# Kernel optimization log

Measured on AMD Instinct MI355X. Metric: run time of the kernel, lower is better.

The kernel has to match this reference:

```python
import jax, jax.numpy as jnp
from jax import lax
import numpy as np
import math

B, T, D_IN, H, L, NDIR = 32, 512, 1024, 512, 2, 2


def setup_inputs() -> dict:
    key = jax.random.key(0)
    ks = jax.random.split(key, 5)
    std = 1.0 / math.sqrt(H)  # torch init: uniform(-std, std)
    u = lambda k, shape: jax.random.uniform(k, shape, jnp.float32, -std, std)
    return {
        "x": jax.random.normal(ks[0], (B, T, D_IN), jnp.float32),
        "Wx": u(ks[1], (L, NDIR, D_IN, 4 * H)),   # x2h weight (in, 4H)
        "bx": u(ks[2], (L, NDIR, 4 * H)),
        "Wh": u(ks[3], (L, NDIR, H, 4 * H)),      # h2h weight (H, 4H)
        "bh": u(ks[4], (L, NDIR, 4 * H)),
    }


def _lstm_dir(xs, Wx, bx, Wh, bh):
    """xs: [T,B,Din]; returns hs [T,B,H], (hT, cT)."""
    # precompute input projection for all timesteps (one big GEMM)
    gx = jnp.einsum('tbd,dg->tbg', xs, Wx) + bx + bh  # [T,B,4H]
    h0 = jnp.zeros((xs.shape[1], Wh.shape[0]), xs.dtype)

    def step(carry, gx_t):
        h, c = carry
        gates = gx_t + h @ Wh  # [B,4H]
        i, f, g, o = jnp.split(gates, 4, axis=-1)  # torch chunk order: i,f,g,o
        i = jax.nn.sigmoid(i)
        f = jax.nn.sigmoid(f)
        g = jnp.tanh(g)
        o = jax.nn.sigmoid(o)
        c = c * f + i * g
        h = o * jnp.tanh(c)
        return (h, c), h

    (hT, cT), hs = lax.scan(step, (h0, h0), gx)
    return hs, hT, cT


def reference(x, Wx, bx, Wh, bh):
    # x: [B,T,D_IN] (batch_first) -> time-major
    inputs = jnp.swapaxes(x, 0, 1)  # [T,B,D]
    h_list, c_list = [], []
    for layer in range(L):
        outs_dirs = []
        for d in range(NDIR):
            xs = inputs if d == 0 else inputs[::-1]
            hs, hT, cT = _lstm_dir(xs, Wx[layer, d], bx[layer, d], Wh[layer, d], bh[layer, d])
            outs_dirs.append(hs if d == 0 else hs[::-1])
            h_list.append(hT)
            c_list.append(cT)
        inputs = jnp.concatenate(outs_dirs, axis=-1)  # [T,B,2H] (dropout=0 / eval)
    output = jnp.swapaxes(inputs, 0, 1)  # [B,T,2H]
    h_n = jnp.stack(h_list)  # [L*NDIR, B, H]
    c_n = jnp.stack(c_list)
    return output, h_n, c_n
```

## Files before the change

### kernel.cpp

```cpp
#include <hip/hip_runtime.h>
#include <hip/hip_bf16.h>

#define DEV __device__ __forceinline__

typedef __bf16 bf16;
typedef __bf16 bf16x8 __attribute__((ext_vector_type(8)));
typedef float f32x4 __attribute__((ext_vector_type(4)));
typedef int i32x4 __attribute__((ext_vector_type(4)));
typedef unsigned int u32;
typedef unsigned long long u64;

#define BB 32
#define TT 512
#define DIN 1024
#define HH 512
#define G4 2048
#define MM (TT*BB)
#define TAGMAGIC 0x5A000000u

DEV float sigmf(float x){ return 1.0f/(1.0f + __expf(-x)); }
DEV float tanhfast(float x){ return 1.0f - 2.0f/(__expf(2.0f*x)+1.0f); }

DEV void gload16(const void* g, void* l){
  __builtin_amdgcn_global_load_lds((const __attribute__((address_space(1))) void*)g,
                                   (__attribute__((address_space(3))) void*)l, 16, 0, 0);
}

DEV i32x4 cload16(const void* p){
  i32x4 v;
  asm volatile("global_load_dwordx4 %0, %1, off sc0 sc1"
               : "=&v"(v) : "v"(p) : "memory");
  return v;
}
DEV void cstore16(void* p, i32x4 v){
  asm volatile("global_store_dwordx4 %0, %1, off sc0 sc1"
               :: "v"(p), "v"(v) : "memory");
}
DEV void waitvm0(){ asm volatile("s_waitcnt vmcnt(0)" ::: "memory"); }

__global__ void k_dbg(float* out, float v){ out[0] = v; }

__global__ void k_prep_bias(const float* __restrict__ bx, const float* __restrict__ bh,
                            float* __restrict__ bsum){
  int gid = blockIdx.x*256 + threadIdx.x;
  if (gid < 4*G4) bsum[gid] = bx[gid] + bh[gid];
}

__global__ void k_xswz(const float* __restrict__ x, bf16* __restrict__ xs){
  int gid = blockIdx.x*256 + threadIdx.x;
  int r = gid >> 7, kc = gid & 127;
  int b = r & 31, t = r >> 5;
  const float* px = x + ((size_t)b*TT + t)*DIN + kc*8;
  float4 v0 = *(const float4*)px;
  float4 v1 = *(const float4*)(px+4);
  bf16x8 o;
  o[0]=(bf16)v0.x; o[1]=(bf16)v0.y; o[2]=(bf16)v0.z; o[3]=(bf16)v0.w;
  o[4]=(bf16)v1.x; o[5]=(bf16)v1.y; o[6]=(bf16)v1.z; o[7]=(bf16)v1.w;
  *(bf16x8*)(xs + (size_t)r*DIN + ((kc ^ (r&7))<<3)) = o;
}

__global__ void k_twx(const float* __restrict__ Wx, bf16* __restrict__ Wxt){
  int ld = blockIdx.z;
  int k0 = blockIdx.x*64, n0 = blockIdx.y*64;
  const float* in = Wx + (size_t)ld*DIN*G4;
  bf16* outp = Wxt + (size_t)ld*G4*DIN;
  __shared__ float tile[64][68];
  int tid = threadIdx.x;
  #pragma unroll
  for (int rr=0; rr<4; rr++){
    int row = rr*16 + (tid>>4); int c4 = (tid&15)*4;
    float4 v = *(const float4*)(in + (size_t)(k0+row)*G4 + n0 + c4);
    *(float4*)&tile[row][c4] = v;
  }
  __syncthreads();
  #pragma unroll
  for (int uu=0; uu<2; uu++){
    int u = uu*256 + tid;
    int nn = u>>3, ck = u&7;
    bf16x8 o;
    #pragma unroll
    for (int j=0;j<8;j++) o[j] = (bf16)tile[ck*8+j][nn];
    int ncol = n0 + nn;
    int kcg = (k0>>3) + ck;
    *(bf16x8*)(outp + (size_t)ncol*DIN + ((size_t)(kcg ^ (ncol&7))<<3)) = o;
  }
}

__global__ void k_twh(const float* __restrict__ Wh, bf16* __restrict__ Whb){
  int ld = blockIdx.z;
  int k0 = blockIdx.x*64, n0 = blockIdx.y*64;
  const float* in = Wh + (size_t)ld*HH*G4;
  bf16* outp = Whb + (size_t)ld*G4*HH;
  __shared__ float tile[64][68];
  int tid = threadIdx.x;
  #pragma unroll
  for (int rr=0; rr<4; rr++){
    int row = rr*16 + (tid>>4); int c4 = (tid&15)*4;
    float4 v = *(const float4*)(in + (size_t)(k0+row)*G4 + n0 + c4);
    *(float4*)&tile[row][c4] = v;
  }
  __syncthreads();
  #pragma unroll
  for (int uu=0; uu<2; uu++){
    int u = uu*256 + tid;
    int nn = u>>3, ck = u&7;
    bf16x8 o;
    #pragma unroll
    for (int j=0;j<8;j++) o[j] = (bf16)tile[ck*8+j][nn];
    int n = n0 + nn;
    int q = n >> 9, rem = n & 511;
    int s = rem >> 4, wq = (rem >> 2) & 3, hcv = rem & 3;
    int cc = s*64 + wq*16 + q*4 + hcv;
    *(bf16x8*)(outp + (size_t)cc*HH + k0 + ck*8) = o;
  }
}

template<typename GXT>
__launch_bounds__(256, 1)
__global__ void k_gemm(const bf16* __restrict__ A, const bf16* __restrict__ Bw,
                       const float* __restrict__ bias, GXT* __restrict__ out){
  int d = blockIdx.z;
  const bf16* Bp = Bw + (size_t)d*G4*DIN;
  const float* bp = bias + d*G4;
  GXT* op = out + (size_t)d*MM*G4;
  int n0 = blockIdx.x*128, r0 = blockIdx.y*128;
  int tid = threadIdx.x, lane = tid&63, w = tid>>6;
  __shared__ __align__(16) bf16 ldsA[128*64];
  __shared__ __align__(16) bf16 ldsB[128*64];
  f32x4 acc[4][4];
  #pragma unroll
  for (int i=0;i<4;i++)
    #pragma unroll
    for (int j=0;j<4;j++) acc[i][j] = (f32x4){0.f,0.f,0.f,0.f};
  int wm = w>>1, wn = w&1;
  for (int kt=0; kt<16; kt++){
    __syncthreads();
    #pragma unroll
    for (int p=0;p<4;p++){
      int seg = p*4 + w;
      int row = seg*8 + (lane>>3);
      int cch = lane&7;
      gload16(A  + (size_t)(r0+row)*DIN + kt*64 + cch*8, ldsA + seg*512);
      gload16(Bp + (size_t)(n0+row)*DIN + kt*64 + cch*8, ldsB + seg*512);
    }
    __syncthreads();
    #pragma unroll
    for (int ks=0; ks<2; ks++){
      bf16x8 af[4], bf_[4];
      #pragma unroll
      for (int at=0; at<4; at++){
        int row = wm*64 + at*16 + (lane&15);
        int ch = (ks*4 + (lane>>4)) ^ (row&7);
        af[at] = *(const bf16x8*)(ldsA + row*64 + ch*8);
      }
      #pragma unroll
      for (int bt=0; bt<4; bt++){
        int col = wn*64 + bt*16 + (lane&15);
        int ch = (ks*4 + (lane>>4)) ^ (col&7);
        bf_[bt] = *(const bf16x8*)(ldsB + col*64 + ch*8);
      }
      #pragma unroll
      for (int at=0; at<4; at++)
        #pragma unroll
        for (int bt=0; bt<4; bt++)
          acc[at][bt] = __builtin_amdgcn_mfma_f32_16x16x32_bf16(af[at], bf_[bt], acc[at][bt], 0,0,0);
    }
  }
  float bv[4];
  #pragma unroll
  for (int bt=0;bt<4;bt++) bv[bt] = bp[n0 + wn*64 + bt*16 + (lane&15)];
  #pragma unroll
  for (int at=0; at<4; at++)
    #pragma unroll
    for (int bt=0; bt<4; bt++)
      #pragma unroll
      for (int rg=0; rg<4; rg++){
        int row = r0 + wm*64 + at*16 + (lane>>4)*4 + rg;
        int col = n0 + wn*64 + bt*16 + (lane&15);
        op[(size_t)row*G4 + col] = (GXT)(acc[at][bt][rg] + bv[bt]);
      }
}

template<typename GXT>
__launch_bounds__(256, 1)
__global__ void k_rec(const bf16* __restrict__ Whb, const GXT* __restrict__ gx,
                      char* __restrict__ hbT,
                      bf16* __restrict__ out0, float* __restrict__ dout,
                      float* __restrict__ hn, float* __restrict__ cn, int layer, int dir0){
  int tid = threadIdx.x, lane = tid&63, w = tid>>6;
  int dl = blockIdx.x >> 5, s = blockIdx.x & 31;
  int d = dir0 + dl;
  __shared__ __align__(16) bf16 hA[32*512];
  __shared__ __align__(8) unsigned short hP[4*128];
  const bf16* Wp = Whb + ((size_t)d*G4 + s*64 + w*16 + (lane&15))*HH;
  bf16x8 bfr[16];
  #pragma unroll
  for (int kk=0; kk<16; kk++) bfr[kk] = *(const bf16x8*)(Wp + kk*32 + (lane>>4)*8);
  float cst[2][4] = {{0,0,0,0},{0,0,0,0}};
  const GXT* gxD = gx + (size_t)dl*MM*G4;
  const u32 tagbase = TAGMAGIC + (u32)((layer*2 + d)*TT);
  int q = (lane>>2)&3, hc = lane&3;
  int colg = q*HH + s*16 + w*4 + hc;
  int m0 = lane&15;
  bool hi = (q >= 2), odd = (q & 1);

  for (int t=0; t<TT; t++){
    int tt = d ? (TT-1-t) : t;
    GXT gxr[2][4];
    {
      const GXT* gp = gxD + (size_t)tt*BB*G4 + colg;
      #pragma unroll
      for (int mt=0; mt<2; mt++)
        #pragma unroll
        for (int rg=0; rg<4; rg++)
          gxr[mt][rg] = gp[(size_t)(mt*16 + (lane>>4)*4 + rg)*G4];
    }
    f32x4 acc0 = {0.f,0.f,0.f,0.f}, acc1 = {0.f,0.f,0.f,0.f};
    if (t > 0){
      const char* sT = hbT + ((size_t)(dl*2 + ((t-1)&1)) << 16);
      u32 want = tagbase + (u32)t;
      i32x4 u[16];
      #pragma unroll
      for (int i=0;i<16;i++){ int g = i*256 + tid; u[i] = cload16(sT + ((size_t)g<<4)); }
      waitvm0();
      __builtin_amdgcn_sched_barrier(0);
      while (true){
        bool bad = false;
        #pragma unroll
        for (int i=0;i<16;i++) bad |= ((u32)u[i].z != want);
        if (!__any(bad)) break;
        __builtin_amdgcn_s_sleep(1);
        #pragma unroll
        for (int i=0;i<16;i++) if ((u32)u[i].z != want){ int g = i*256 + tid; u[i] = cload16(sT + ((size_t)g<<4)); }
        waitvm0();
        __builtin_amdgcn_sched_barrier(0);
      }
      __syncthreads();
      #pragma unroll
      for (int i=0;i<16;i++){
        int g = i*256 + tid; int b = g>>7, cu = g&127;
        u64 dat = ((u64)(u32)u[i].y << 32) | (u32)u[i].x;
        *(u64*)((char*)hA + b*1024 + ((((cu>>1) ^ (b&7)))<<4) + (cu&1)*8) = dat;
      }
      __syncthreads();
      #pragma unroll
      for (int kk=0; kk<16; kk++){
        int ch = (kk*4 + (lane>>4)) ^ (m0&7);
        bf16x8 a0 = *(const bf16x8*)(hA + m0*HH + ch*8);
        bf16x8 a1 = *(const bf16x8*)(hA + (m0+16)*HH + ch*8);
        acc0 = __builtin_amdgcn_mfma_f32_16x16x32_bf16(a0, bfr[kk], acc0, 0,0,0);
        acc1 = __builtin_amdgcn_mfma_f32_16x16x32_bf16(a1, bfr[kk], acc1, 0,0,0);
      }
    }
    #pragma unroll
    for (int mt=0; mt<2; mt++){
      #pragma unroll
      for (int rg=0; rg<4; rg++){
        float gpre = (mt ? acc1[rg] : acc0[rg]) + (float)gxr[mt][rg];
        float x4  = __shfl_xor(gpre, 4);
        float x8  = __shfl_xor(gpre, 8);
        float x12 = __shfl_xor(gpre, 12);
        float a04 = odd ? x4 : gpre,  b04 = odd ? gpre : x4;
        float a812 = odd ? x12 : x8,  b812 = odd ? x8 : x12;
        float ig = hi ? a812 : a04;
        float fg = hi ? b812 : b04;
        float gg = hi ? a04 : a812;
        float og = hi ? b04 : b812;
        float iv = sigmf(ig), fv = sigmf(fg), gv = tanhfast(gg), ov = sigmf(og);
        float c = cst[mt][rg]*fv + iv*gv;
        cst[mt][rg] = c;
        float hvv = ov * tanhfast(c);
        if (q == 0){
          int b = mt*16 + (lane>>4)*4 + rg;
          hP[w*128 + b*4 + hc] = __builtin_bit_cast(unsigned short, (bf16)hvv);
          if (layer == 1)
            __builtin_nontemporal_store(hvv,
              dout + ((size_t)(b*TT + tt))*(2*HH) + d*HH + s*16 + w*4 + hc);
          if (t == TT-1)
            hn[((size_t)((layer*2+d)*BB + b))*HH + s*16 + w*4 + hc] = hvv;
        }
      }
    }
    if (t == TT-1 && q == 0){
      #pragma unroll
      for (int mt=0; mt<2; mt++)
        #pragma unroll
        for (int rg=0; rg<4; rg++){
          int b = mt*16 + (lane>>4)*4 + rg;
          cn[((size_t)((layer*2+d)*BB + b))*HH + s*16 + w*4 + hc] = cst[mt][rg];
        }
    }
    if (lane < 32){
      u64 d8 = *(const u64*)(hP + w*128 + lane*4);
      if (t < TT-1){
        char* dT = hbT + ((size_t)(dl*2 + (t&1)) << 16);
        i32x4 unit;
        unit.x = (int)(u32)(d8 & 0xffffffffu);
        unit.y = (int)(u32)(d8 >> 32);
        unit.z = (int)(tagbase + (u32)t + 1u);
        unit.w = 0;
        cstore16(dT + ((size_t)(lane*128 + s*4 + w) << 4), unit);
      }
      if (layer == 0){
        int r = tt*BB + lane;
        int c = d*64 + s*2 + (w>>1);
        *(u64*)(out0 + (size_t)r*DIN + (size_t)(c ^ (r&7))*8 + (w&1)*4) = d8;
      }
    }
  }
}

extern "C" void kernel_launch(void* const* d_in, const int* in_sizes, int n_in,
                              void* d_out, int out_size, void* d_ws, size_t ws_size,
                              hipStream_t stream){
  const float* x  = (const float*)d_in[0];
  const float* Wx = (const float*)d_in[1];
  const float* bx = (const float*)d_in[2];
  const float* Wh = (const float*)d_in[3];
  const float* bh = (const float*)d_in[4];
  float* outp = (float*)d_out;
  char* ws = (char*)d_ws;

  const size_t szWxt  = (size_t)4*G4*DIN*2;
  const size_t szWhb  = (size_t)4*G4*HH*2;
  const size_t szBsum = (size_t)4*G4*4;
  const size_t szXO   = (size_t)MM*DIN*2;
  const size_t szHbT  = (size_t)2*2*4096*16;

  int mode = -1;
  size_t oWxt=0,oWhb=0,oBsum=0,oXO=0,oOut0=0,oHbT=0,oGx=0;
  for (int m=0; m<3 && mode<0; m++){
    size_t off = 0;
    auto take = [&](size_t b)->size_t{ size_t r = off; off = (off + b + 255) & ~(size_t)255; return r; };
    oWxt = take(szWxt); oWhb = take(szWhb); oBsum = take(szBsum);
    oXO  = take(szXO);
    oOut0 = (m==2) ? take(szXO) : oXO;
    oHbT = take(szHbT);
    size_t gxb = (m==0) ? (size_t)2*MM*G4*4 : (m==1) ? (size_t)2*MM*G4*2 : (size_t)MM*G4*2;
    oGx = take(gxb);
    if (off <= ws_size) mode = m;
  }
  if (mode < 0){
    k_dbg<<<1, 1, 0, stream>>>(outp, (float)((double)ws_size / 1048576.0));
    return;
  }

  bf16* Wxt  = (bf16*)(ws + oWxt);
  bf16* Whb  = (bf16*)(ws + oWhb);
  float* bsum= (float*)(ws + oBsum);
  bf16* xo   = (bf16*)(ws + oXO);
  bf16* out0 = (bf16*)(ws + oOut0);
  char* hbT  = ws + oHbT;
  void* gxp  = (void*)(ws + oGx);

  float* hn = outp + (size_t)BB*TT*2*HH;
  float* cn = hn + (size_t)4*BB*HH;

  hipMemsetAsync(hbT, 0, szHbT, stream);
  k_prep_bias<<<32, 256, 0, stream>>>(bx, bh, bsum);
  k_xswz<<<(MM*128)/256, 256, 0, stream>>>(x, xo);
  k_twx<<<dim3(16,32,4), 256, 0, stream>>>(Wx, Wxt);
  k_twh<<<dim3(8,32,4), 256, 0, stream>>>(Wh, Whb);

  if (mode == 0){
    float* gx = (float*)gxp;
    for (int layer=0; layer<2; layer++){
      k_gemm<float><<<dim3(16,128,2), 256, 0, stream>>>(xo, Wxt + (size_t)layer*2*G4*DIN,
                                                        bsum + layer*2*G4, gx);
      k_rec<float><<<64, 256, 0, stream>>>(Whb + (size_t)layer*2*G4*HH, gx, hbT,
                                           out0, outp, hn, cn, layer, 0);
    }
  } else if (mode == 1){
    bf16* gx = (bf16*)gxp;
    for (int layer=0; layer<2; layer++){
      k_gemm<bf16><<<dim3(16,128,2), 256, 0, stream>>>(xo, Wxt + (size_t)layer*2*G4*DIN,
                                                       bsum + layer*2*G4, gx);
      k_rec<bf16><<<64, 256, 0, stream>>>(Whb + (size_t)layer*2*G4*HH, gx, hbT,
                                          out0, outp, hn, cn, layer, 0);
    }
  } else {
    bf16* gx = (bf16*)gxp;
    for (int layer=0; layer<2; layer++){
      const bf16* A = layer ? out0 : xo;
      for (int dd=0; dd<2; dd++){
        k_gemm<bf16><<<dim3(16,128,1), 256, 0, stream>>>(A, Wxt + (size_t)(layer*2+dd)*G4*DIN,
                                                         bsum + (layer*2+dd)*G4, gx);
        k_rec<bf16><<<32, 256, 0, stream>>>(Whb + (size_t)layer*2*G4*HH, gx, hbT,
                                            out0, outp, hn, cn, layer, dd);
      }
    }
  }
}
```

Before: 5.624 ms.

## Process both LSTM directions in one recurrent block, interleaved per timestep

The recurrent kernel now launches 32 blocks, each handling one slice of both directions, instead of 64 blocks with one direction each. Per timestep a block spins on direction 0's h exchange, computes and publishes it, then does the same for direction 1. Ideally each direction's inter-block sync latency is hidden behind the other direction's compute. This doubles the weight registers per thread and serializes both directions' work within one CU. The fallback mode that ran one direction per launch is also removed.

```diff
diff --git a/kernel.cpp b/kernel.cpp
--- a/kernel.cpp
+++ b/kernel.cpp
@@ -183,128 +183,136 @@
 
 template<typename GXT>
 __launch_bounds__(256, 1)
-__global__ void k_rec(const bf16* __restrict__ Whb, const GXT* __restrict__ gx,
-                      char* __restrict__ hbT,
-                      bf16* __restrict__ out0, float* __restrict__ dout,
-                      float* __restrict__ hn, float* __restrict__ cn, int layer, int dir0){
+__global__ void k_rec2(const bf16* __restrict__ Whb, const GXT* __restrict__ gx,
+                       char* __restrict__ hbT,
+                       bf16* __restrict__ out0, float* __restrict__ dout,
+                       float* __restrict__ hn, float* __restrict__ cn, int layer){
   int tid = threadIdx.x, lane = tid&63, w = tid>>6;
-  int dl = blockIdx.x >> 5, s = blockIdx.x & 31;
-  int d = dir0 + dl;
+  int s = blockIdx.x;
   __shared__ __align__(16) bf16 hA[32*512];
   __shared__ __align__(8) unsigned short hP[4*128];
-  const bf16* Wp = Whb + ((size_t)d*G4 + s*64 + w*16 + (lane&15))*HH;
-  bf16x8 bfr[16];
-  #pragma unroll
-  for (int kk=0; kk<16; kk++) bfr[kk] = *(const bf16x8*)(Wp + kk*32 + (lane>>4)*8);
-  float cst[2][4] = {{0,0,0,0},{0,0,0,0}};
-  const GXT* gxD = gx + (size_t)dl*MM*G4;
-  const u32 tagbase = TAGMAGIC + (u32)((layer*2 + d)*TT);
+  bf16x8 bfr[2][16];
+  #pragma unroll
+  for (int d=0; d<2; d++){
+    const bf16* Wp = Whb + ((size_t)d*G4 + s*64 + w*16 + (lane&15))*HH;
+    #pragma unroll
+    for (int kk=0; kk<16; kk++) bfr[d][kk] = *(const bf16x8*)(Wp + kk*32 + (lane>>4)*8);
+  }
+  float cst[2][2][4] = {};
   int q = (lane>>2)&3, hc = lane&3;
   int colg = q*HH + s*16 + w*4 + hc;
   int m0 = lane&15;
   bool hi = (q >= 2), odd = (q & 1);
+  u32 tagb0 = TAGMAGIC + (u32)((layer*2+0)*TT);
+  u32 tagb1 = TAGMAGIC + (u32)((layer*2+1)*TT);
 
   for (int t=0; t<TT; t++){
-    int tt = d ? (TT-1-t) : t;
-    GXT gxr[2][4];
-    {
-      const GXT* gp = gxD + (size_t)tt*BB*G4 + colg;
+    GXT gxr[2][2][4];
+    #pragma unroll
+    for (int d=0; d<2; d++){
+      int tt = d ? (TT-1-t) : t;
+      const GXT* gp = gx + (size_t)d*MM*G4 + (size_t)tt*BB*G4 + colg;
       #pragma unroll
       for (int mt=0; mt<2; mt++)
         #pragma unroll
         for (int rg=0; rg<4; rg++)
-          gxr[mt][rg] = gp[(size_t)(mt*16 + (lane>>4)*4 + rg)*G4];
-    }
-    f32x4 acc0 = {0.f,0.f,0.f,0.f}, acc1 = {0.f,0.f,0.f,0.f};
-    if (t > 0){
-      const char* sT = hbT + ((size_t)(dl*2 + ((t-1)&1)) << 16);
-      u32 want = tagbase + (u32)t;
-      i32x4 u[16];
-      #pragma unroll
-      for (int i=0;i<16;i++){ int g = i*256 + tid; u[i] = cload16(sT + ((size_t)g<<4)); }
-      waitvm0();
-      __builtin_amdgcn_sched_barrier(0);
-      while (true){
-        bool bad = false;
-        #pragma unroll
-        for (int i=0;i<16;i++) bad |= ((u32)u[i].z != want);
-        if (!__any(bad)) break;
-        __builtin_amdgcn_s_sleep(1);
-        #pragma unroll
-        for (int i=0;i<16;i++) if ((u32)u[i].z != want){ int g = i*256 + tid; u[i] = cload16(sT + ((size_t)g<<4)); }
+          gxr[d][mt][rg] = gp[(size_t)(mt*16 + (lane>>4)*4 + rg)*G4];
+    }
+    #pragma unroll
+    for (int d=0; d<2; d++){
+      int tt = d ? (TT-1-t) : t;
+      u32 tagbase = d ? tagb1 : tagb0;
+      f32x4 acc0 = {0.f,0.f,0.f,0.f}, acc1 = {0.f,0.f,0.f,0.f};
+      if (t > 0){
+        const char* sT = hbT + ((size_t)(d*2 + ((t-1)&1)) << 16);
+        u32 want = tagbase + (u32)t;
+        i32x4 u[16];
+        #pragma unroll
+        for (int i=0;i<16;i++){ int g = i*256 + tid; u[i] = cload16(sT + ((size_t)g<<4)); }
         waitvm0();
         __builtin_amdgcn_sched_barrier(0);
-      }
-      __syncthreads();
-      #pragma unroll
-      for (int i=0;i<16;i++){
-        int g = i*256 + tid; int b = g>>7, cu = g&127;
-        u64 dat = ((u64)(u32)u[i].y << 32) | (u32)u[i].x;
-        *(u64*)((char*)hA + b*1024 + ((((cu>>1) ^ (b&7)))<<4) + (cu&1)*8) = dat;
-      }
-      __syncthreads();
-      #pragma unroll
-      for (int kk=0; kk<16; kk++){
-        int ch = (kk*4 + (lane>>4)) ^ (m0&7);
-        bf16x8 a0 = *(const bf16x8*)(hA + m0*HH + ch*8);
-        bf16x8 a1 = *(const bf16x8*)(hA + (m0+16)*HH + ch*8);
-        acc0 = __builtin_amdgcn_mfma_f32_16x16x32_bf16(a0, bfr[kk], acc0, 0,0,0);
-        acc1 = __builtin_amdgcn_mfma_f32_16x16x32_bf16(a1, bfr[kk], acc1, 0,0,0);
-      }
-    }
-    #pragma unroll
-    for (int mt=0; mt<2; mt++){
-      #pragma unroll
-      for (int rg=0; rg<4; rg++){
-        float gpre = (mt ? acc1[rg] : acc0[rg]) + (float)gxr[mt][rg];
-        float x4  = __shfl_xor(gpre, 4);
-        float x8  = __shfl_xor(gpre, 8);
-        float x12 = __shfl_xor(gpre, 12);
-        float a04 = odd ? x4 : gpre,  b04 = odd ? gpre : x4;
-        float a812 = odd ? x12 : x8,  b812 = odd ? x8 : x12;
-        float ig = hi ? a812 : a04;
-        float fg = hi ? b812 : b04;
-        float gg = hi ? a04 : a812;
-        float og = hi ? b04 : b812;
-        float iv = sigmf(ig), fv = sigmf(fg), gv = tanhfast(gg), ov = sigmf(og);
-        float c = cst[mt][rg]*fv + iv*gv;
-        cst[mt][rg] = c;
-        float hvv = ov * tanhfast(c);
-        if (q == 0){
-          int b = mt*16 + (lane>>4)*4 + rg;
-          hP[w*128 + b*4 + hc] = __builtin_bit_cast(unsigned short, (bf16)hvv);
-          if (layer == 1)
-            __builtin_nontemporal_store(hvv,
-              dout + ((size_t)(b*TT + tt))*(2*HH) + d*HH + s*16 + w*4 + hc);
-          if (t == TT-1)
-            hn[((size_t)((layer*2+d)*BB + b))*HH + s*16 + w*4 + hc] = hvv;
-        }
-      }
-    }
-    if (t == TT-1 && q == 0){
-      #pragma unroll
-      for (int mt=0; mt<2; mt++)
+        while (true){
+          bool bad = false;
+          #pragma unroll
+          for (int i=0;i<16;i++) bad |= ((u32)u[i].z != want);
+          if (!__any(bad)) break;
+          __builtin_amdgcn_s_sleep(1);
+          #pragma unroll
+          for (int i=0;i<16;i++) if ((u32)u[i].z != want){ int g = i*256 + tid; u[i] = cload16(sT + ((size_t)g<<4)); }
+          waitvm0();
+          __builtin_amdgcn_sched_barrier(0);
+        }
+        __syncthreads();
+        #pragma unroll
+        for (int i=0;i<16;i++){
+          int g = i*256 + tid; int b = g>>7, cu = g&127;
+          u64 dat = ((u64)(u32)u[i].y << 32) | (u32)u[i].x;
+          *(u64*)((char*)hA + b*1024 + ((((cu>>1) ^ (b&7)))<<4) + (cu&1)*8) = dat;
+        }
+        __syncthreads();
+        #pragma unroll
+        for (int kk=0; kk<16; kk++){
+          int ch = (kk*4 + (lane>>4)) ^ (m0&7);
+          bf16x8 a0 = *(const bf16x8*)(hA + m0*HH + ch*8);
+          bf16x8 a1 = *(const bf16x8*)(hA + (m0+16)*HH + ch*8);
+          acc0 = __builtin_amdgcn_mfma_f32_16x16x32_bf16(a0, bfr[d][kk], acc0, 0,0,0);
+          acc1 = __builtin_amdgcn_mfma_f32_16x16x32_bf16(a1, bfr[d][kk], acc1, 0,0,0);
+        }
+      }
+      #pragma unroll
+      for (int mt=0; mt<2; mt++){
         #pragma unroll
         for (int rg=0; rg<4; rg++){
-          int b = mt*16 + (lane>>4)*4 + rg;
-          cn[((size_t)((layer*2+d)*BB + b))*HH + s*16 + w*4 + hc] = cst[mt][rg];
-        }
-    }
-    if (lane < 32){
-      u64 d8 = *(const u64*)(hP + w*128 + lane*4);
-      if (t < TT-1){
-        char* dT = hbT + ((size_t)(dl*2 + (t&1)) << 16);
-        i32x4 unit;
-        unit.x = (int)(u32)(d8 & 0xffffffffu);
-        unit.y = (int)(u32)(d8 >> 32);
-        unit.z = (int)(tagbase + (u32)t + 1u);
-        unit.w = 0;
-        cstore16(dT + ((size_t)(lane*128 + s*4 + w) << 4), unit);
-      }
-      if (layer == 0){
-        int r = tt*BB + lane;
-        int c = d*64 + s*2 + (w>>1);
-        *(u64*)(out0 + (size_t)r*DIN + (size_t)(c ^ (r&7))*8 + (w&1)*4) = d8;
+          float gpre = (mt ? acc1[rg] : acc0[rg]) + (float)gxr[d][mt][rg];
+          float x4  = __shfl_xor(gpre, 4);
+          float x8  = __shfl_xor(gpre, 8);
+          float x12 = __shfl_xor(gpre, 12);
+          float a04 = odd ? x4 : gpre,  b04 = odd ? gpre : x4;
+          float a812 = odd ? x12 : x8,  b812 = odd ? x8 : x12;
+          float ig = hi ? a812 : a04;
+          float fg = hi ? b812 : b04;
+          float gg = hi ? a04 : a812;
+          float og = hi ? b04 : b812;
+          float iv = sigmf(ig), fv = sigmf(fg), gv = tanhfast(gg), ov = sigmf(og);
+          float c = cst[d][mt][rg]*fv + iv*gv;
+          cst[d][mt][rg] = c;
+          float hvv = ov * tanhfast(c);
+          if (q == 0){
+            int b = mt*16 + (lane>>4)*4 + rg;
+            hP[w*128 + b*4 + hc] = __builtin_bit_cast(unsigned short, (bf16)hvv);
+            if (layer == 1)
+              __builtin_nontemporal_store(hvv,
+                dout + ((size_t)(b*TT + tt))*(2*HH) + d*HH + s*16 + w*4 + hc);
+            if (t == TT-1)
+              hn[((size_t)((layer*2+d)*BB + b))*HH + s*16 + w*4 + hc] = hvv;
+          }
+        }
+      }
+      if (t == TT-1 && q == 0){
+        #pragma unroll
+        for (int mt=0; mt<2; mt++)
+          #pragma unroll
+          for (int rg=0; rg<4; rg++){
+            int b = mt*16 + (lane>>4)*4 + rg;
+            cn[((size_t)((layer*2+d)*BB + b))*HH + s*16 + w*4 + hc] = cst[d][mt][rg];
+          }
+      }
+      if (lane < 32){
+        u64 d8 = *(const u64*)(hP + w*128 + lane*4);
+        if (t < TT-1){
+          char* dT = hbT + ((size_t)(d*2 + (t&1)) << 16);
+          i32x4 unit;
+          unit.x = (int)(u32)(d8 & 0xffffffffu);
+          unit.y = (int)(u32)(d8 >> 32);
+          unit.z = (int)(tagbase + (u32)t + 1u);
+          unit.w = 0;
+          cstore16(dT + ((size_t)(lane*128 + s*4 + w) << 4), unit);
+        }
+        if (layer == 0){
+          int r = tt*BB + lane;
+          int c = d*64 + s*2 + (w>>1);
+          *(u64*)(out0 + (size_t)r*DIN + (size_t)(c ^ (r&7))*8 + (w&1)*4) = d8;
+        }
       }
     }
   }
@@ -328,15 +336,14 @@
   const size_t szHbT  = (size_t)2*2*4096*16;
 
   int mode = -1;
-  size_t oWxt=0,oWhb=0,oBsum=0,oXO=0,oOut0=0,oHbT=0,oGx=0;
-  for (int m=0; m<3 && mode<0; m++){
+  size_t oWxt=0,oWhb=0,oBsum=0,oXO=0,oHbT=0,oGx=0;
+  for (int m=0; m<2 && mode<0; m++){
     size_t off = 0;
     auto take = [&](size_t b)->size_t{ size_t r = off; off = (off + b + 255) & ~(size_t)255; return r; };
     oWxt = take(szWxt); oWhb = take(szWhb); oBsum = take(szBsum);
     oXO  = take(szXO);
-    oOut0 = (m==2) ? take(szXO) : oXO;
     oHbT = take(szHbT);
-    size_t gxb = (m==0) ? (size_t)2*MM*G4*4 : (m==1) ? (size_t)2*MM*G4*2 : (size_t)MM*G4*2;
+    size_t gxb = (m==0) ? (size_t)2*MM*G4*4 : (size_t)2*MM*G4*2;
     oGx = take(gxb);
     if (off <= ws_size) mode = m;
   }
@@ -349,7 +356,7 @@
   bf16* Whb  = (bf16*)(ws + oWhb);
   float* bsum= (float*)(ws + oBsum);
   bf16* xo   = (bf16*)(ws + oXO);
-  bf16* out0 = (bf16*)(ws + oOut0);
+  bf16* out0 = xo;
   char* hbT  = ws + oHbT;
   void* gxp  = (void*)(ws + oGx);
 
@@ -367,27 +374,16 @@
     for (int layer=0; layer<2; layer++){
       k_gemm<float><<<dim3(16,128,2), 256, 0, stream>>>(xo, Wxt + (size_t)layer*2*G4*DIN,
                                                         bsum + layer*2*G4, gx);
-      k_rec<float><<<64, 256, 0, stream>>>(Whb + (size_t)layer*2*G4*HH, gx, hbT,
-                                           out0, outp, hn, cn, layer, 0);
-    }
-  } else if (mode == 1){
+      k_rec2<float><<<32, 256, 0, stream>>>(Whb + (size_t)layer*2*G4*HH, gx, hbT,
+                                            out0, outp, hn, cn, layer);
+    }
+  } else {
     bf16* gx = (bf16*)gxp;
     for (int layer=0; layer<2; layer++){
       k_gemm<bf16><<<dim3(16,128,2), 256, 0, stream>>>(xo, Wxt + (size_t)layer*2*G4*DIN,
                                                        bsum + layer*2*G4, gx);
-      k_rec<bf16><<<64, 256, 0, stream>>>(Whb + (size_t)layer*2*G4*HH, gx, hbT,
-                                          out0, outp, hn, cn, layer, 0);
-    }
-  } else {
-    bf16* gx = (bf16*)gxp;
-    for (int layer=0; layer<2; layer++){
-      const bf16* A = layer ? out0 : xo;
-      for (int dd=0; dd<2; dd++){
-        k_gemm<bf16><<<dim3(16,128,1), 256, 0, stream>>>(A, Wxt + (size_t)(layer*2+dd)*G4*DIN,
-                                                         bsum + (layer*2+dd)*G4, gx);
-        k_rec<bf16><<<32, 256, 0, stream>>>(Whb + (size_t)layer*2*G4*HH, gx, hbT,
-                                            out0, outp, hn, cn, layer, dd);
-      }
-    }
-  }
-}
+      k_rec2<bf16><<<32, 256, 0, stream>>>(Whb + (size_t)layer*2*G4*HH, gx, hbT,
+                                           out0, outp, hn, cn, layer);
+    }
+  }
+}
```

Result: slower. 10.02 ms (+78.2%).

## Store gate projections in recurrence-native packed bf16 layout and drop fallback modes

Applied to the files above, without the earlier changes.

The input-projection GEMM now writes its bf16 output in a permuted layout that matches how each recurrent block and thread consumes gates. Each thread in the recurrence can then fetch its eight gate values per step with one 16-byte load instead of eight strided scalar loads. The workspace-size fallback modes (fp32 gx, per-direction launches) are removed, so bf16 gx with both directions per launch is always used. This cuts per-step load latency on the serial critical path but requires enough workspace.

```diff
diff --git a/kernel.cpp b/kernel.cpp
--- a/kernel.cpp
+++ b/kernel.cpp
@@ -115,14 +115,13 @@
   }
 }
 
-template<typename GXT>
 __launch_bounds__(256, 1)
-__global__ void k_gemm(const bf16* __restrict__ A, const bf16* __restrict__ Bw,
-                       const float* __restrict__ bias, GXT* __restrict__ out){
+__global__ void k_gemmp(const bf16* __restrict__ A, const bf16* __restrict__ Bw,
+                        const float* __restrict__ bias, bf16* __restrict__ out){
   int d = blockIdx.z;
   const bf16* Bp = Bw + (size_t)d*G4*DIN;
   const float* bp = bias + d*G4;
-  GXT* op = out + (size_t)d*MM*G4;
+  bf16* op = out + (size_t)d*MM*G4;
   int n0 = blockIdx.x*128, r0 = blockIdx.y*128;
   int tid = threadIdx.x, lane = tid&63, w = tid>>6;
   __shared__ __align__(16) bf16 ldsA[128*64];
@@ -169,27 +168,33 @@
   float bv[4];
   #pragma unroll
   for (int bt=0;bt<4;bt++) bv[bt] = bp[n0 + wn*64 + bt*16 + (lane&15)];
-  #pragma unroll
-  for (int at=0; at<4; at++)
-    #pragma unroll
-    for (int bt=0; bt<4; bt++)
-      #pragma unroll
-      for (int rg=0; rg<4; rg++){
-        int row = r0 + wm*64 + at*16 + (lane>>4)*4 + rg;
-        int col = n0 + wn*64 + bt*16 + (lane&15);
-        op[(size_t)row*G4 + col] = (GXT)(acc[at][bt][rg] + bv[bt]);
-      }
-}
-
-template<typename GXT>
+  int l4 = lane>>4;
+  #pragma unroll
+  for (int a=0; a<2; a++){
+    int tt = (r0 + wm*64 + a*32) >> 5;
+    #pragma unroll
+    for (int bt=0; bt<4; bt++){
+      int col = n0 + wn*64 + bt*16 + (lane&15);
+      int q = col >> 9, rem = col & 511;
+      int sD = rem >> 4, wR = (rem >> 2) & 3, hcD = rem & 3;
+      int tIdx = wR*64 + l4*16 + q*4 + hcD;
+      bf16x8 u8;
+      #pragma unroll
+      for (int j=0;j<4;j++) u8[j]   = (bf16)(acc[a*2][bt][j]   + bv[bt]);
+      #pragma unroll
+      for (int j=0;j<4;j++) u8[4+j] = (bf16)(acc[a*2+1][bt][j] + bv[bt]);
+      *(bf16x8*)(op + (((size_t)tt*32 + sD)*256 + tIdx)*8) = u8;
+    }
+  }
+}
+
 __launch_bounds__(256, 1)
-__global__ void k_rec(const bf16* __restrict__ Whb, const GXT* __restrict__ gx,
+__global__ void k_rec(const bf16* __restrict__ Whb, const bf16* __restrict__ gx,
                       char* __restrict__ hbT,
                       bf16* __restrict__ out0, float* __restrict__ dout,
-                      float* __restrict__ hn, float* __restrict__ cn, int layer, int dir0){
+                      float* __restrict__ hn, float* __restrict__ cn, int layer){
   int tid = threadIdx.x, lane = tid&63, w = tid>>6;
-  int dl = blockIdx.x >> 5, s = blockIdx.x & 31;
-  int d = dir0 + dl;
+  int d = blockIdx.x >> 5, s = blockIdx.x & 31;
   __shared__ __align__(16) bf16 hA[32*512];
   __shared__ __align__(8) unsigned short hP[4*128];
   const bf16* Wp = Whb + ((size_t)d*G4 + s*64 + w*16 + (lane&15))*HH;
@@ -197,27 +202,18 @@
   #pragma unroll
   for (int kk=0; kk<16; kk++) bfr[kk] = *(const bf16x8*)(Wp + kk*32 + (lane>>4)*8);
   float cst[2][4] = {{0,0,0,0},{0,0,0,0}};
-  const GXT* gxD = gx + (size_t)dl*MM*G4;
+  const bf16* gxD = gx + (size_t)d*MM*G4;
   const u32 tagbase = TAGMAGIC + (u32)((layer*2 + d)*TT);
   int q = (lane>>2)&3, hc = lane&3;
-  int colg = q*HH + s*16 + w*4 + hc;
   int m0 = lane&15;
   bool hi = (q >= 2), odd = (q & 1);
 
   for (int t=0; t<TT; t++){
     int tt = d ? (TT-1-t) : t;
-    GXT gxr[2][4];
-    {
-      const GXT* gp = gxD + (size_t)tt*BB*G4 + colg;
-      #pragma unroll
-      for (int mt=0; mt<2; mt++)
-        #pragma unroll
-        for (int rg=0; rg<4; rg++)
-          gxr[mt][rg] = gp[(size_t)(mt*16 + (lane>>4)*4 + rg)*G4];
-    }
+    bf16x8 gv = *(const bf16x8*)(gxD + (((size_t)tt*32 + s)*256 + tid)*8);
     f32x4 acc0 = {0.f,0.f,0.f,0.f}, acc1 = {0.f,0.f,0.f,0.f};
     if (t > 0){
-      const char* sT = hbT + ((size_t)(dl*2 + ((t-1)&1)) << 16);
+      const char* sT = hbT + ((size_t)(d*2 + ((t-1)&1)) << 16);
       u32 want = tagbase + (u32)t;
       i32x4 u[16];
       #pragma unroll
@@ -256,7 +252,7 @@
     for (int mt=0; mt<2; mt++){
       #pragma unroll
       for (int rg=0; rg<4; rg++){
-        float gpre = (mt ? acc1[rg] : acc0[rg]) + (float)gxr[mt][rg];
+        float gpre = (mt ? acc1[rg] : acc0[rg]) + (float)gv[mt*4+rg];
         float x4  = __shfl_xor(gpre, 4);
         float x8  = __shfl_xor(gpre, 8);
         float x12 = __shfl_xor(gpre, 12);
@@ -266,8 +262,8 @@
         float fg = hi ? b812 : b04;
         float gg = hi ? a04 : a812;
         float og = hi ? b04 : b812;
-        float iv = sigmf(ig), fv = sigmf(fg), gv = tanhfast(gg), ov = sigmf(og);
-        float c = cst[mt][rg]*fv + iv*gv;
+        float iv = sigmf(ig), fv = sigmf(fg), gv_ = tanhfast(gg), ov = sigmf(og);
+        float c = cst[mt][rg]*fv + iv*gv_;
         cst[mt][rg] = c;
         float hvv = ov * tanhfast(c);
         if (q == 0){
@@ -293,7 +289,7 @@
     if (lane < 32){
       u64 d8 = *(const u64*)(hP + w*128 + lane*4);
       if (t < TT-1){
-        char* dT = hbT + ((size_t)(dl*2 + (t&1)) << 16);
+        char* dT = hbT + ((size_t)(d*2 + (t&1)) << 16);
         i32x4 unit;
         unit.x = (int)(u32)(d8 & 0xffffffffu);
         unit.y = (int)(u32)(d8 >> 32);
@@ -326,21 +322,13 @@
   const size_t szBsum = (size_t)4*G4*4;
   const size_t szXO   = (size_t)MM*DIN*2;
   const size_t szHbT  = (size_t)2*2*4096*16;
-
-  int mode = -1;
-  size_t oWxt=0,oWhb=0,oBsum=0,oXO=0,oOut0=0,oHbT=0,oGx=0;
-  for (int m=0; m<3 && mode<0; m++){
-    size_t off = 0;
-    auto take = [&](size_t b)->size_t{ size_t r = off; off = (off + b + 255) & ~(size_t)255; return r; };
-    oWxt = take(szWxt); oWhb = take(szWhb); oBsum = take(szBsum);
-    oXO  = take(szXO);
-    oOut0 = (m==2) ? take(szXO) : oXO;
-    oHbT = take(szHbT);
-    size_t gxb = (m==0) ? (size_t)2*MM*G4*4 : (m==1) ? (size_t)2*MM*G4*2 : (size_t)MM*G4*2;
-    oGx = take(gxb);
-    if (off <= ws_size) mode = m;
-  }
-  if (mode < 0){
+  const size_t szGx   = (size_t)2*MM*G4*2;
+
+  size_t off = 0;
+  auto take = [&](size_t b)->size_t{ size_t r = off; off = (off + b + 255) & ~(size_t)255; return r; };
+  size_t oWxt = take(szWxt), oWhb = take(szWhb), oBsum = take(szBsum);
+  size_t oXO  = take(szXO), oHbT = take(szHbT), oGx = take(szGx);
+  if (off > ws_size){
     k_dbg<<<1, 1, 0, stream>>>(outp, (float)((double)ws_size / 1048576.0));
     return;
   }
@@ -349,9 +337,9 @@
   bf16* Whb  = (bf16*)(ws + oWhb);
   float* bsum= (float*)(ws + oBsum);
   bf16* xo   = (bf16*)(ws + oXO);
-  bf16* out0 = (bf16*)(ws + oOut0);
+  bf16* out0 = xo;
   char* hbT  = ws + oHbT;
-  void* gxp  = (void*)(ws + oGx);
+  bf16* gx   = (bf16*)(ws + oGx);
 
   float* hn = outp + (size_t)BB*TT*2*HH;
   float* cn = hn + (size_t)4*BB*HH;
@@ -362,32 +350,10 @@
   k_twx<<<dim3(16,32,4), 256, 0, stream>>>(Wx, Wxt);
   k_twh<<<dim3(8,32,4), 256, 0, stream>>>(Wh, Whb);
 
-  if (mode == 0){
-    float* gx = (float*)gxp;
-    for (int layer=0; layer<2; layer++){
-      k_gemm<float><<<dim3(16,128,2), 256, 0, stream>>>(xo, Wxt + (size_t)layer*2*G4*DIN,
-                                                        bsum + layer*2*G4, gx);
-      k_rec<float><<<64, 256, 0, stream>>>(Whb + (size_t)layer*2*G4*HH, gx, hbT,
-                                           out0, outp, hn, cn, layer, 0);
-    }
-  } else if (mode == 1){
-    bf16* gx = (bf16*)gxp;
-    for (int layer=0; layer<2; layer++){
-      k_gemm<bf16><<<dim3(16,128,2), 256, 0, stream>>>(xo, Wxt + (size_t)layer*2*G4*DIN,
-                                                       bsum + layer*2*G4, gx);
-      k_rec<bf16><<<64, 256, 0, stream>>>(Whb + (size_t)layer*2*G4*HH, gx, hbT,
-                                          out0, outp, hn, cn, layer, 0);
-    }
-  } else {
-    bf16* gx = (bf16*)gxp;
-    for (int layer=0; layer<2; layer++){
-      const bf16* A = layer ? out0 : xo;
-      for (int dd=0; dd<2; dd++){
-        k_gemm<bf16><<<dim3(16,128,1), 256, 0, stream>>>(A, Wxt + (size_t)(layer*2+dd)*G4*DIN,
-                                                         bsum + (layer*2+dd)*G4, gx);
-        k_rec<bf16><<<32, 256, 0, stream>>>(Whb + (size_t)layer*2*G4*HH, gx, hbT,
-                                            out0, outp, hn, cn, layer, dd);
-      }
-    }
-  }
-}
+  for (int layer=0; layer<2; layer++){
+    k_gemmp<<<dim3(16,128,2), 256, 0, stream>>>(xo, Wxt + (size_t)layer*2*G4*DIN,
+                                                bsum + layer*2*G4, gx);
+    k_rec<<<64, 256, 0, stream>>>(Whb + (size_t)layer*2*G4*HH, gx, hbT,
+                                  out0, outp, hn, cn, layer);
+  }
+}
```

Result: slower. 5.766 ms (+2.5%).
